# Kernel optimization log

Measured on AMD Instinct MI355X. Metric: run time of the kernel, lower is better.

The kernel has to match this reference:

```python
import jax, jax.numpy as jnp
import numpy as np


def setup_inputs() -> dict:
    key = jax.random.key(0)
    k1, k2, k3 = jax.random.split(key, 3)
    B, T, D = 64, 256, 512
    real = jax.random.normal(k1, (B, T, D), dtype=jnp.float32)
    imag = jax.random.normal(k2, (B, T, D), dtype=jnp.float32)
    weight = jax.random.uniform(k3, (B, T, 1), dtype=jnp.float32)
    return {"real": real, "imag": imag, "weight": weight}


def reference(real, imag, weight):
    # Weighted complex outer-product mixture:
    #   out_r[b] = sum_t w[b,t] * (r_t r_t^T + i_t i_t^T)
    #   out_i[b] = sum_t w[b,t] * (i_t r_t^T - r_t i_t^T)
    # Equivalent to the original per-sample loop + TxDxD outer products,
    # but fused: scale one operand by w and contract over t directly.
    w = weight[..., 0]  # [B, T]
    rw = real * w[..., None]  # [B, T, D]
    iw = imag * w[..., None]
    out_r = jnp.einsum('btd,bte->bde', rw, real) + jnp.einsum('btd,bte->bde', iw, imag)
    out_i = jnp.einsum('btd,bte->bde', iw, real) - jnp.einsum('btd,bte->bde', rw, imag)
    return (out_r, out_i)
```

## Files before the change

### kernel.cpp

```cpp
#include <hip/hip_runtime.h>
#include <cstdint>
#include <cstddef>

#define BB 64
#define TT 256
#define DD 512
#define BK 32
#define TILEM 128

typedef short bf16x8 __attribute__((ext_vector_type(8)));
typedef float f32x4  __attribute__((ext_vector_type(4)));
typedef int   i32x4  __attribute__((ext_vector_type(4)));

static __device__ __forceinline__ unsigned short f2bf(float x) {
  unsigned u = __builtin_bit_cast(unsigned, x) + 0x8000u;
  return (unsigned short)(u >> 16);
}

__global__ __launch_bounds__(256, 2)
void ComplexMixture_54838142435828_kernel(const float* __restrict__ re,
                                          const float* __restrict__ im,
                                          const float* __restrict__ wt,
                                          float* __restrict__ out) {
  __shared__ __attribute__((aligned(16))) unsigned short sAr[4 * 128 * 8];
  __shared__ __attribute__((aligned(16))) unsigned short sAi[4 * 128 * 8];
  __shared__ __attribute__((aligned(16))) unsigned short sBr[4 * 128 * 8];
  __shared__ __attribute__((aligned(16))) unsigned short sBi[4 * 128 * 8];
  __shared__ float sw[TT];

  const int tid = threadIdx.x;

  const int L = blockIdx.x;
  const int c = L & 7;
  const int s = L >> 3;
  const int b  = c * 8 + (s >> 4);
  const int t5 = s & 15;
  const int d0 = (t5 >> 2) * TILEM;
  const int e0 = (t5 & 3) * TILEM;

  sw[tid] = wt[b * TT + tid];

  const int lane = tid & 63;
  const int wid  = tid >> 6;
  const int wm = (wid >> 1) * 64;
  const int wn = (wid & 1) * 64;
  const int quad = lane >> 4;
  const int l16  = lane & 15;

  f32x4 accR[4][4], accI[4][4];
  #pragma unroll
  for (int mt = 0; mt < 4; ++mt)
    #pragma unroll
    for (int nt = 0; nt < 4; ++nt) {
      accR[mt][nt] = (f32x4){0.f, 0.f, 0.f, 0.f};
      accI[mt][nt] = (f32x4){0.f, 0.f, 0.f, 0.f};
    }

  const int sd = tid & 127;
  const int kh = tid >> 7;

  for (int kt = 0; kt < TT; kt += BK) {
    __syncthreads();

    const int kb = kt + kh * 16;
    const size_t rowBase = ((size_t)(b * TT + kb)) * DD;

    {
      const float* pr = re + rowBase + d0 + sd;
      const float* pi = im + rowBase + d0 + sd;
      #pragma unroll
      for (int cc = 0; cc < 2; ++cc) {
        union { unsigned short h[8]; i32x4 q; } ur, ui;
        #pragma unroll
        for (int j = 0; j < 8; ++j) {
          const int k = cc * 8 + j;
          const float wv = sw[kb + k];
          ur.h[j] = f2bf(pr[(size_t)k * DD] * wv);
          ui.h[j] = f2bf(pi[(size_t)k * DD] * wv);
        }
        const int off = ((kh * 2 + cc) * 128 + sd) * 8;
        *(i32x4*)&sAr[off] = ur.q;
        *(i32x4*)&sAi[off] = ui.q;
      }
    }
    {
      const float* qr = re + rowBase + e0 + sd;
      const float* qi = im + rowBase + e0 + sd;
      #pragma unroll
      for (int cc = 0; cc < 2; ++cc) {
        union { unsigned short h[8]; i32x4 q; } ur, ui;
        #pragma unroll
        for (int j = 0; j < 8; ++j) {
          const int k = cc * 8 + j;
          ur.h[j] = f2bf(qr[(size_t)k * DD]);
          ui.h[j] = f2bf(qi[(size_t)k * DD]);
        }
        const int off = ((kh * 2 + cc) * 128 + sd) * 8;
        *(i32x4*)&sBr[off] = ur.q;
        *(i32x4*)&sBi[off] = ui.q;
      }
    }
    __syncthreads();

    bf16x8 aR[4], aI[4], bR[4], bI[4];
    #pragma unroll
    for (int t = 0; t < 4; ++t) {
      const int offA = (quad * 128 + wm + t * 16 + l16) * 8;
      const int offB = (quad * 128 + wn + t * 16 + l16) * 8;
      aR[t] = *(const bf16x8*)&sAr[offA];
      aI[t] = *(const bf16x8*)&sAi[offA];
      bR[t] = *(const bf16x8*)&sBr[offB];
      bI[t] = *(const bf16x8*)&sBi[offB];
    }
    #pragma unroll
    for (int mt = 0; mt < 4; ++mt) {
      const bf16x8 aRn = aR[mt] ^ (bf16x8)((short)0x8000);
      #pragma unroll
      for (int nt = 0; nt < 4; ++nt) {
        accR[mt][nt] = __builtin_amdgcn_mfma_f32_16x16x32_bf16(aR[mt], bR[nt], accR[mt][nt], 0, 0, 0);
        accR[mt][nt] = __builtin_amdgcn_mfma_f32_16x16x32_bf16(aI[mt], bI[nt], accR[mt][nt], 0, 0, 0);
        accI[mt][nt] = __builtin_amdgcn_mfma_f32_16x16x32_bf16(aI[mt], bR[nt], accI[mt][nt], 0, 0, 0);
        accI[mt][nt] = __builtin_amdgcn_mfma_f32_16x16x32_bf16(aRn,    bI[nt], accI[mt][nt], 0, 0, 0);
      }
    }
  }

  const size_t NOFF = (size_t)BB * DD * DD;
  #pragma unroll
  for (int mt = 0; mt < 4; ++mt) {
    #pragma unroll
    for (int r = 0; r < 4; ++r) {
      const int drow = d0 + wm + mt * 16 + quad * 4 + r;
      const size_t rowOff = ((size_t)(b * DD + drow)) * DD;
      #pragma unroll
      for (int nt = 0; nt < 4; ++nt) {
        const int ecol = e0 + wn + nt * 16 + l16;
        out[rowOff + ecol]        = accR[mt][nt][r];
        out[NOFF + rowOff + ecol] = accI[mt][nt][r];
      }
    }
  }
}

extern "C" void kernel_launch(void* const* d_in, const int* in_sizes, int n_in,
                              void* d_out, int out_size, void* d_ws, size_t ws_size,
                              hipStream_t stream) {
  const float* re = (const float*)d_in[0];
  const float* im = (const float*)d_in[1];
  const float* wt = (const float*)d_in[2];
  float* out = (float*)d_out;
  ComplexMixture_54838142435828_kernel<<<dim3(1024), dim3(256), 0, stream>>>(re, im, wt, out);
}
```

Before: 213.9 us.

## Exploit output symmetry: compute upper-triangle tiles and write transposed mirror

Because out_r is symmetric and out_i is antisymmetric, the kernel now launches only the 10 upper-triangular 128x128 tiles per batch instead of 16. Off-diagonal tiles also write their transpose, negated for the imaginary part, staged through shared memory so the stores are coalesced. Output stores become nontemporal. This cuts the MFMA and input-load work by about 37% but adds an LDS transpose pass with extra syncs, and the output write traffic stays the same.

Measured after the change: 339.1 us. 58.6% more time.

```diff
diff --git a/kernel.cpp b/kernel.cpp
--- a/kernel.cpp
+++ b/kernel.cpp
@@ -22,21 +22,24 @@
                                           const float* __restrict__ im,
                                           const float* __restrict__ wt,
                                           float* __restrict__ out) {
-  __shared__ __attribute__((aligned(16))) unsigned short sAr[4 * 128 * 8];
-  __shared__ __attribute__((aligned(16))) unsigned short sAi[4 * 128 * 8];
-  __shared__ __attribute__((aligned(16))) unsigned short sBr[4 * 128 * 8];
-  __shared__ __attribute__((aligned(16))) unsigned short sBi[4 * 128 * 8];
-  __shared__ float sw[TT];
+  __shared__ __attribute__((aligned(16))) char smem[33792];
+  unsigned short* sAr = (unsigned short*)(smem);
+  unsigned short* sAi = (unsigned short*)(smem + 8192);
+  unsigned short* sBr = (unsigned short*)(smem + 16384);
+  unsigned short* sBi = (unsigned short*)(smem + 24576);
+  float*          sw  = (float*)(smem + 32768);
 
   const int tid = threadIdx.x;
 
   const int L = blockIdx.x;
   const int c = L & 7;
   const int s = L >> 3;
-  const int b  = c * 8 + (s >> 4);
-  const int t5 = s & 15;
-  const int d0 = (t5 >> 2) * TILEM;
-  const int e0 = (t5 & 3) * TILEM;
+  const int b  = c * 8 + s / 10;
+  const int t  = s % 10;
+  const int ti = (t >= 6) ? 3 : (t >= 3) ? 2 : (t >= 1) ? 1 : 0;
+  const int tj = t - ((ti * (ti + 1)) >> 1);
+  const int d0 = ti * TILEM;
+  const int e0 = tj * TILEM;
 
   sw[tid] = wt[b * TT + tid];
 
@@ -104,13 +107,13 @@
 
     bf16x8 aR[4], aI[4], bR[4], bI[4];
     #pragma unroll
-    for (int t = 0; t < 4; ++t) {
-      const int offA = (quad * 128 + wm + t * 16 + l16) * 8;
-      const int offB = (quad * 128 + wn + t * 16 + l16) * 8;
-      aR[t] = *(const bf16x8*)&sAr[offA];
-      aI[t] = *(const bf16x8*)&sAi[offA];
-      bR[t] = *(const bf16x8*)&sBr[offB];
-      bI[t] = *(const bf16x8*)&sBi[offB];
+    for (int tt = 0; tt < 4; ++tt) {
+      const int offA = (quad * 128 + wm + tt * 16 + l16) * 8;
+      const int offB = (quad * 128 + wn + tt * 16 + l16) * 8;
+      aR[tt] = *(const bf16x8*)&sAr[offA];
+      aI[tt] = *(const bf16x8*)&sAi[offA];
+      bR[tt] = *(const bf16x8*)&sBr[offB];
+      bI[tt] = *(const bf16x8*)&sBi[offB];
     }
     #pragma unroll
     for (int mt = 0; mt < 4; ++mt) {
@@ -135,8 +138,34 @@
       #pragma unroll
       for (int nt = 0; nt < 4; ++nt) {
         const int ecol = e0 + wn + nt * 16 + l16;
-        out[rowOff + ecol]        = accR[mt][nt][r];
-        out[NOFF + rowOff + ecol] = accI[mt][nt][r];
+        __builtin_nontemporal_store(accR[mt][nt][r], &out[rowOff + ecol]);
+        __builtin_nontemporal_store(accI[mt][nt][r], &out[NOFF + rowOff + ecol]);
+      }
+    }
+  }
+
+  if (ti != tj) {
+    float* tbR = (float*)(smem + wid * 8192);
+    float* tbI = tbR + 1024;
+    #pragma unroll
+    for (int mt = 0; mt < 4; ++mt) {
+      __syncthreads();
+      #pragma unroll
+      for (int nt = 0; nt < 4; ++nt) {
+        const int col = nt * 16 + l16;
+        *(f32x4*)&tbR[col * 16 + quad * 4] = accR[mt][nt];
+        const f32x4 vi = accI[mt][nt];
+        *(f32x4*)&tbI[col * 16 + quad * 4] = (f32x4){-vi[0], -vi[1], -vi[2], -vi[3]};
+      }
+      __syncthreads();
+      const size_t trOff = ((size_t)(b * DD + e0 + wn + lane)) * DD
+                         + (size_t)(d0 + wm + mt * 16);
+      #pragma unroll
+      for (int j = 0; j < 4; ++j) {
+        const f32x4 vr = *(const f32x4*)&tbR[lane * 16 + j * 4];
+        const f32x4 vi = *(const f32x4*)&tbI[lane * 16 + j * 4];
+        __builtin_nontemporal_store(vr, (f32x4*)&out[trOff + j * 4]);
+        __builtin_nontemporal_store(vi, (f32x4*)&out[NOFF + trOff + j * 4]);
       }
     }
   }
@@ -149,5 +178,5 @@
   const float* im = (const float*)d_in[1];
   const float* wt = (const float*)d_in[2];
   float* out = (float*)d_out;
-  ComplexMixture_54838142435828_kernel<<<dim3(1024), dim3(256), 0, stream>>>(re, im, wt, out);
+  ComplexMixture_54838142435828_kernel<<<dim3(640), dim3(256), 0, stream>>>(re, im, wt, out);
 }
```
